# Performance work log

Hardware: AMD Instinct MI355X
Metric: run time of the kernel (lower is better)

## Reference

```python
import jax, jax.numpy as jnp
import numpy as np

B, N, C = 4, 1024, 1024
H, D = 16, 64            # n_heads, head_dim; inner_dim = H*D = C
L = 6                    # n_blocks
FF = 4 * C
SCALE = C ** (-0.5)      # source uses width**-0.5
EPS = 1e-5


def setup_inputs() -> dict:
    key = jax.random.key(0)
    ks = jax.random.split(key, 9)
    s = 0.02
    return {
        "x":     jax.random.normal(ks[0], (B, N, C), dtype=jnp.float32),
        "Wqkv":  jax.random.normal(ks[1], (L, C, 3 * H * D), dtype=jnp.float32) * s,
        "Wout":  jax.random.normal(ks[2], (L, H * D, C), dtype=jnp.float32) * s,
        "bout":  jnp.zeros((L, C), dtype=jnp.float32),
        "W1":    jax.random.normal(ks[3], (L, C, FF), dtype=jnp.float32) * s,
        "b1":    jnp.zeros((L, FF), dtype=jnp.float32),
        "W2":    jax.random.normal(ks[4], (L, FF, C), dtype=jnp.float32) * s,
        "b2":    jnp.zeros((L, C), dtype=jnp.float32),
        "ln1_g": jnp.ones((C,), dtype=jnp.float32),
        "ln1_b": jnp.zeros((C,), dtype=jnp.float32),
        "ln2_g": jnp.ones((C,), dtype=jnp.float32),
        "ln2_b": jnp.zeros((C,), dtype=jnp.float32),
    }


def _layernorm(y, g, b):
    mu = jnp.mean(y, axis=-1, keepdims=True)
    var = jnp.mean(jnp.square(y - mu), axis=-1, keepdims=True)
    return (y - mu) * jax.lax.rsqrt(var + EPS) * g + b


def reference(x, Wqkv, Wout, bout, W1, b1, W2, b2, ln1_g, ln1_b, ln2_g, ln2_b):
    for l in range(L):
        # --- pre-norm multi-head attention (shared LN params across blocks) ---
        h = _layernorm(x, ln1_g, ln1_b)
        qkv = h @ Wqkv[l]                              # [B,N,3HD]
        q, k, v = jnp.split(qkv, 3, axis=-1)
        def heads(t):
            return t.reshape(B, N, H, D).transpose(0, 2, 1, 3)  # [B,H,N,D]
        q, k, v = heads(q), heads(k), heads(v)
        dots = jnp.einsum('bhid,bhjd->bhij', q, k) * SCALE
        attn = jax.nn.softmax(dots, axis=-1)
        o = jnp.einsum('bhij,bhjd->bhid', attn, v)     # [B,H,N,D]
        o = o.transpose(0, 2, 1, 3).reshape(B, N, H * D)
        x = x + (o @ Wout[l] + bout[l])
        # --- pre-norm FFN with exact GELU ---
        h2 = _layernorm(x, ln2_g, ln2_b)
        f = jax.nn.gelu(h2 @ W1[l] + b1[l], approximate=False) @ W2[l] + b2[l]
        x = x + f
    return x
```

## Files before the change

kernel.cpp:

```cpp
#include <hip/hip_runtime.h>
#include <stdint.h>

typedef unsigned short u16;
typedef __bf16  bf16x8 __attribute__((ext_vector_type(8)));
typedef float   f32x4  __attribute__((ext_vector_type(4)));

#define DEVINL __device__ __forceinline__

DEVINL u16 f2bf(float f) {
    union { float f; uint32_t u; } v; v.f = f;
    uint32_t r = v.u + 0x7fffu + ((v.u >> 16) & 1u);
    return (u16)(r >> 16);
}

DEVINL float gelu_exact(float x) {
    return 0.5f * x * (1.0f + erff(x * 0.70710678118654752f));
}

typedef const void __attribute__((address_space(1))) gvoid;
typedef void __attribute__((address_space(3))) lvoid;
DEVINL void gload_lds16(const u16* g, u16* l) {
    __builtin_amdgcn_global_load_lds((gvoid*)g, (lvoid*)l, 16, 0, 0);
}

__global__ __launch_bounds__(256) void k_transpose_conv(
    const float* __restrict__ W, u16* __restrict__ Wt, int K, int N) {
    __shared__ float t[32][33];
    const int n0 = blockIdx.x * 32, k0 = blockIdx.y * 32;
    const int tx = threadIdx.x & 31, ty = threadIdx.x >> 5;
#pragma unroll
    for (int i = 0; i < 4; i++)
        t[ty + i * 8][tx] = W[(size_t)(k0 + ty + i * 8) * N + n0 + tx];
    __syncthreads();
#pragma unroll
    for (int i = 0; i < 4; i++)
        Wt[(size_t)(n0 + ty + i * 8) * K + k0 + tx] = f2bf(t[tx][ty + i * 8]);
}

__global__ __launch_bounds__(256) void k_layernorm(
    const float* __restrict__ x, const float* __restrict__ g,
    const float* __restrict__ b, u16* __restrict__ out) {
    const int row = blockIdx.x, tid = threadIdx.x;
    float4 v = ((const float4*)x)[(size_t)row * 256 + tid];
    float s  = v.x + v.y + v.z + v.w;
    float s2 = v.x * v.x + v.y * v.y + v.z * v.z + v.w * v.w;
#pragma unroll
    for (int off = 32; off > 0; off >>= 1) {
        s  += __shfl_down(s, off);
        s2 += __shfl_down(s2, off);
    }
    __shared__ float rs[4], rs2[4];
    const int wv = tid >> 6;
    if ((tid & 63) == 0) { rs[wv] = s; rs2[wv] = s2; }
    __syncthreads();
    s  = rs[0] + rs[1] + rs[2] + rs[3];
    s2 = rs2[0] + rs2[1] + rs2[2] + rs2[3];
    const float mu  = s * (1.0f / 1024.0f);
    const float var = s2 * (1.0f / 1024.0f) - mu * mu;
    const float rstd = rsqrtf(var + 1e-5f);
    float4 gv = ((const float4*)g)[tid];
    float4 bv = ((const float4*)b)[tid];
    uint2 o;
    u16 a0 = f2bf((v.x - mu) * rstd * gv.x + bv.x);
    u16 a1 = f2bf((v.y - mu) * rstd * gv.y + bv.y);
    u16 a2 = f2bf((v.z - mu) * rstd * gv.z + bv.z);
    u16 a3 = f2bf((v.w - mu) * rstd * gv.w + bv.w);
    o.x = a0 | ((uint32_t)a1 << 16);
    o.y = a2 | ((uint32_t)a3 << 16);
    ((uint2*)out)[(size_t)row * 256 + tid] = o;
}

enum { EPI_BF16 = 0, EPI_F32_BIAS_RES = 1, EPI_BF16_BIAS_GELU = 2 };

template <int EPI>
__global__ __launch_bounds__(256) void k_gemm_bt(
    const u16* __restrict__ A, const u16* __restrict__ Bt,
    void* outp, const float* __restrict__ bias, const float* res,
    int N, int K) {
    __shared__ __align__(16) u16 As[128 * 32];
    __shared__ __align__(16) u16 Bs[128 * 32];
    const int tid  = threadIdx.x;
    const int lane = tid & 63, wv = tid >> 6;
    const int wm = wv >> 1, wn = wv & 1;
    const int lr = lane >> 2, lc = (lane & 3) * 8;
    const int c0 = wv * 2;
    const size_t aRow0 = (size_t)blockIdx.y * 128;
    const size_t bRow0 = (size_t)blockIdx.x * 128;

    f32x4 acc[4][4] = {};
    const int mrow = lane & 15;
    const int koff = (lane >> 4) * 8;
    const int kIters = K >> 5;

    for (int kt = 0; kt < kIters; kt++) {
        const int k0 = kt << 5;
        gload_lds16(A  + (aRow0 + (size_t)(c0 * 16      + lr)) * K + k0 + lc, &As[c0 * 512]);
        gload_lds16(A  + (aRow0 + (size_t)(c0 * 16 + 16 + lr)) * K + k0 + lc, &As[(c0 + 1) * 512]);
        gload_lds16(Bt + (bRow0 + (size_t)(c0 * 16      + lr)) * K + k0 + lc, &Bs[c0 * 512]);
        gload_lds16(Bt + (bRow0 + (size_t)(c0 * 16 + 16 + lr)) * K + k0 + lc, &Bs[(c0 + 1) * 512]);
        __syncthreads();
        bf16x8 af[4], bfv[4];
#pragma unroll
        for (int i = 0; i < 4; i++)
            af[i] = *(const bf16x8*)&As[(wm * 64 + i * 16 + mrow) * 32 + koff];
#pragma unroll
        for (int i = 0; i < 4; i++)
            bfv[i] = *(const bf16x8*)&Bs[(wn * 64 + i * 16 + mrow) * 32 + koff];
#pragma unroll
        for (int mi = 0; mi < 4; mi++)
#pragma unroll
            for (int ni = 0; ni < 4; ni++)
                acc[mi][ni] = __builtin_amdgcn_mfma_f32_16x16x32_bf16(
                    af[mi], bfv[ni], acc[mi][ni], 0, 0, 0);
        __syncthreads();
    }

    const int rr = (lane >> 4) * 4;
    const int cc = lane & 15;
#pragma unroll
    for (int mi = 0; mi < 4; mi++) {
#pragma unroll
        for (int ni = 0; ni < 4; ni++) {
#pragma unroll
            for (int r = 0; r < 4; r++) {
                const size_t row = aRow0 + wm * 64 + mi * 16 + rr + r;
                const size_t col = bRow0 + wn * 64 + ni * 16 + cc;
                const float v = acc[mi][ni][r];
                if (EPI == EPI_BF16) {
                    ((u16*)outp)[row * N + col] = f2bf(v);
                } else if (EPI == EPI_F32_BIAS_RES) {
                    ((float*)outp)[row * N + col] = res[row * N + col] + v + bias[col];
                } else {
                    ((u16*)outp)[row * N + col] = f2bf(gelu_exact(v + bias[col]));
                }
            }
        }
    }
}

__global__ __launch_bounds__(256) void k_vtrans(
    const u16* __restrict__ qkv, u16* __restrict__ vT) {
    __shared__ u16 t[32][33];
    const int bh = blockIdx.z;
    const int b = bh >> 4, h = bh & 15;
    const int n0 = blockIdx.x * 32, d0 = blockIdx.y * 32;
    const int tx = threadIdx.x & 31, ty = threadIdx.x >> 5;
#pragma unroll
    for (int i = 0; i < 4; i++)
        t[ty + i * 8][tx] = qkv[(size_t)(b * 1024 + n0 + ty + i * 8) * 3072 + 2048 + h * 64 + d0 + tx];
    __syncthreads();
#pragma unroll
    for (int i = 0; i < 4; i++)
        vT[(size_t)(bh * 64 + d0 + ty + i * 8) * 1024 + n0 + tx] = t[tx][ty + i * 8];
}

__global__ __launch_bounds__(256) void k_attention(
    const u16* __restrict__ qkv, const u16* __restrict__ vT, u16* __restrict__ o) {
    const int qt = blockIdx.x, h = blockIdx.y, b = blockIdx.z;
    const int tid = threadIdx.x;
    const int lane = tid & 63, wv = tid >> 6;
    const int quad = lane >> 4, l16 = lane & 15;
    __shared__ __align__(16) u16 Ks[64 * 64];
    __shared__ __align__(16) u16 Vs[64 * 64];
    __shared__ __align__(16) u16 Ps[4][16 * 64];
    const int q0 = qt * 64 + wv * 16;

    bf16x8 qa[2];
    {
        const u16* qp = qkv + (size_t)(b * 1024 + q0 + l16) * 3072 + h * 64 + quad * 8;
        qa[0] = *(const bf16x8*)qp;
        qa[1] = *(const bf16x8*)(qp + 32);
    }
    f32x4 oacc[4] = {};
    float mst[4], lst[4];
#pragma unroll
    for (int r = 0; r < 4; r++) { mst[r] = -__builtin_inff(); lst[r] = 0.f; }

    const int tr = tid >> 3, tc = (tid & 7) * 8;
    const size_t kvbase = (size_t)(b * 1024) * 3072 + 1024 + h * 64;
    const size_t vtbase = (size_t)(b * 16 + h) * 64 * 1024;

    for (int j0 = 0; j0 < 1024; j0 += 64) {
        *(uint4*)&Ks[tr * 64 + tc]        = *(const uint4*)&qkv[kvbase + (size_t)(j0 + tr) * 3072 + tc];
        *(uint4*)&Ks[(tr + 32) * 64 + tc] = *(const uint4*)&qkv[kvbase + (size_t)(j0 + tr + 32) * 3072 + tc];
        *(uint4*)&Vs[tr * 64 + tc]        = *(const uint4*)&vT[vtbase + (size_t)tr * 1024 + j0 + tc];
        *(uint4*)&Vs[(tr + 32) * 64 + tc] = *(const uint4*)&vT[vtbase + (size_t)(tr + 32) * 1024 + j0 + tc];
        __syncthreads();

        f32x4 s[4] = {};
#pragma unroll
        for (int nt = 0; nt < 4; nt++) {
            bf16x8 kb0 = *(const bf16x8*)&Ks[(nt * 16 + l16) * 64 + quad * 8];
            bf16x8 kb1 = *(const bf16x8*)&Ks[(nt * 16 + l16) * 64 + quad * 8 + 32];
            s[nt] = __builtin_amdgcn_mfma_f32_16x16x32_bf16(qa[0], kb0, s[nt], 0, 0, 0);
            s[nt] = __builtin_amdgcn_mfma_f32_16x16x32_bf16(qa[1], kb1, s[nt], 0, 0, 0);
        }
#pragma unroll
        for (int r = 0; r < 4; r++) {
            float v0 = s[0][r] * 0.03125f, v1 = s[1][r] * 0.03125f;
            float v2 = s[2][r] * 0.03125f, v3 = s[3][r] * 0.03125f;
            float mx = fmaxf(fmaxf(v0, v1), fmaxf(v2, v3));
#pragma unroll
            for (int off = 1; off < 16; off <<= 1) mx = fmaxf(mx, __shfl_xor(mx, off));
            const float mnew = fmaxf(mst[r], mx);
            const float alpha = __expf(mst[r] - mnew);
            mst[r] = mnew;
            const float p0 = __expf(v0 - mnew), p1 = __expf(v1 - mnew);
            const float p2 = __expf(v2 - mnew), p3 = __expf(v3 - mnew);
            float rsum = p0 + p1 + p2 + p3;
#pragma unroll
            for (int off = 1; off < 16; off <<= 1) rsum += __shfl_xor(rsum, off);
            lst[r] = lst[r] * alpha + rsum;
#pragma unroll
            for (int dt = 0; dt < 4; dt++) oacc[dt][r] *= alpha;
            u16* pr = &Ps[wv][(quad * 4 + r) * 64 + l16];
            pr[0]  = f2bf(p0); pr[16] = f2bf(p1);
            pr[32] = f2bf(p2); pr[48] = f2bf(p3);
        }
        __syncthreads();
        bf16x8 pa0 = *(const bf16x8*)&Ps[wv][l16 * 64 + quad * 8];
        bf16x8 pa1 = *(const bf16x8*)&Ps[wv][l16 * 64 + quad * 8 + 32];
#pragma unroll
        for (int dt = 0; dt < 4; dt++) {
            bf16x8 vb0 = *(const bf16x8*)&Vs[(dt * 16 + l16) * 64 + quad * 8];
            bf16x8 vb1 = *(const bf16x8*)&Vs[(dt * 16 + l16) * 64 + quad * 8 + 32];
            oacc[dt] = __builtin_amdgcn_mfma_f32_16x16x32_bf16(pa0, vb0, oacc[dt], 0, 0, 0);
            oacc[dt] = __builtin_amdgcn_mfma_f32_16x16x32_bf16(pa1, vb1, oacc[dt], 0, 0, 0);
        }
        __syncthreads();
    }
#pragma unroll
    for (int dt = 0; dt < 4; dt++)
#pragma unroll
        for (int r = 0; r < 4; r++) {
            const float v = oacc[dt][r] / lst[r];
            o[(size_t)(b * 1024 + q0 + quad * 4 + r) * 1024 + h * 64 + dt * 16 + l16] = f2bf(v);
        }
}

extern "C" void kernel_launch(void* const* d_in, const int* in_sizes, int n_in,
                              void* d_out, int out_size, void* d_ws, size_t ws_size,
                              hipStream_t stream) {
    const float* x_in = (const float*)d_in[0];
    const float* Wqkv = (const float*)d_in[1];
    const float* Wout = (const float*)d_in[2];
    const float* bout = (const float*)d_in[3];
    const float* W1   = (const float*)d_in[4];
    const float* b1   = (const float*)d_in[5];
    const float* W2   = (const float*)d_in[6];
    const float* b2   = (const float*)d_in[7];
    const float* ln1g = (const float*)d_in[8];
    const float* ln1b = (const float*)d_in[9];
    const float* ln2g = (const float*)d_in[10];
    const float* ln2b = (const float*)d_in[11];
    float* xbuf = (float*)d_out;

    char* p = (char*)d_ws;
    auto carve = [&](size_t elems) -> u16* {
        u16* r = (u16*)p;
        p += ((elems * 2 + 255) & ~(size_t)255);
        return r;
    };
    u16* wq   = carve((size_t)3072 * 1024);
    u16* wo   = carve((size_t)1024 * 1024);
    u16* w1t  = carve((size_t)4096 * 1024);
    u16* w2t  = carve((size_t)1024 * 4096);
    u16* hb   = carve((size_t)4096 * 1024);
    u16* qkvb = carve((size_t)4096 * 3072);
    u16* vtb  = carve((size_t)4096 * 1024);
    u16* ob   = carve((size_t)4096 * 1024);
    u16* gb   = carve((size_t)4096 * 4096);
    if ((size_t)(p - (char*)d_ws) > ws_size) return;

    hipMemcpyAsync(xbuf, x_in, (size_t)4096 * 1024 * 4, hipMemcpyDeviceToDevice, stream);

    for (int l = 0; l < 6; l++) {
        k_transpose_conv<<<dim3(96, 32), 256, 0, stream>>>(Wqkv + (size_t)l * 1024 * 3072, wq, 1024, 3072);
        k_transpose_conv<<<dim3(32, 32), 256, 0, stream>>>(Wout + (size_t)l * 1024 * 1024, wo, 1024, 1024);
        k_transpose_conv<<<dim3(128, 32), 256, 0, stream>>>(W1 + (size_t)l * 1024 * 4096, w1t, 1024, 4096);
        k_transpose_conv<<<dim3(32, 128), 256, 0, stream>>>(W2 + (size_t)l * 4096 * 1024, w2t, 4096, 1024);

        k_layernorm<<<4096, 256, 0, stream>>>(xbuf, ln1g, ln1b, hb);
        k_gemm_bt<EPI_BF16><<<dim3(24, 32), 256, 0, stream>>>(hb, wq, qkvb, nullptr, nullptr, 3072, 1024);
        k_vtrans<<<dim3(32, 2, 64), 256, 0, stream>>>(qkvb, vtb);
        k_attention<<<dim3(16, 16, 4), 256, 0, stream>>>(qkvb, vtb, ob);
        k_gemm_bt<EPI_F32_BIAS_RES><<<dim3(8, 32), 256, 0, stream>>>(ob, wo, xbuf, bout + (size_t)l * 1024, xbuf, 1024, 1024);
        k_layernorm<<<4096, 256, 0, stream>>>(xbuf, ln2g, ln2b, hb);
        k_gemm_bt<EPI_BF16_BIAS_GELU><<<dim3(32, 32), 256, 0, stream>>>(hb, w1t, gb, b1 + (size_t)l * 4096, nullptr, 4096, 1024);
        k_gemm_bt<EPI_F32_BIAS_RES><<<dim3(8, 32), 256, 0, stream>>>(gb, w2t, xbuf, b2 + (size_t)l * 1024, xbuf, 1024, 4096);
    }
}
```

Before: 2.394 ms.

## Split-K with atomic residual add for narrow GEMMs, swizzle LDS tiles

The N=1024 GEMMs (attention output projection and FFN down projection) are split along K across blockIdx.z, 2 and 4 ways. Each split atomically adds its partial into the fp32 residual buffer, and split 0 also adds the bias. This raises the grid from 256 blocks to 512/1024 so more CUs are busy. Separately, the GEMM and attention LDS tiles use XOR swizzles and a padded P buffer to cut bank conflicts. In exchange, fp32 atomics add memory traffic and make the summation order nondeterministic.

```diff
diff --git a/kernel.cpp b/kernel.cpp
--- a/kernel.cpp
+++ b/kernel.cpp
@@ -70,30 +70,34 @@
     ((uint2*)out)[(size_t)row * 256 + tid] = o;
 }
 
-enum { EPI_BF16 = 0, EPI_F32_BIAS_RES = 1, EPI_BF16_BIAS_GELU = 2 };
+enum { EPI_BF16 = 0, EPI_F32_ATOMIC = 1, EPI_BF16_BIAS_GELU = 2 };
 
 template <int EPI>
 __global__ __launch_bounds__(256) void k_gemm_bt(
     const u16* __restrict__ A, const u16* __restrict__ Bt,
-    void* outp, const float* __restrict__ bias, const float* res,
-    int N, int K) {
+    void* outp, const float* __restrict__ bias,
+    int N, int K, int kPer) {
     __shared__ __align__(16) u16 As[128 * 32];
     __shared__ __align__(16) u16 Bs[128 * 32];
     const int tid  = threadIdx.x;
     const int lane = tid & 63, wv = tid >> 6;
     const int wm = wv >> 1, wn = wv & 1;
-    const int lr = lane >> 2, lc = (lane & 3) * 8;
+    const int lr = lane >> 2;
+    const int lc = ((lane & 3) ^ ((lane >> 3) & 3)) * 8;
     const int c0 = wv * 2;
     const size_t aRow0 = (size_t)blockIdx.y * 128;
     const size_t bRow0 = (size_t)blockIdx.x * 128;
+    const int ks = blockIdx.z;
+    const int kBase = ks * kPer;
 
     f32x4 acc[4][4] = {};
     const int mrow = lane & 15;
-    const int koff = (lane >> 4) * 8;
-    const int kIters = K >> 5;
+    const int quad = lane >> 4;
+    const int koff = ((quad ^ ((mrow >> 1) & 3)) << 3);
+    const int kIters = kPer >> 5;
 
     for (int kt = 0; kt < kIters; kt++) {
-        const int k0 = kt << 5;
+        const int k0 = kBase + (kt << 5);
         gload_lds16(A  + (aRow0 + (size_t)(c0 * 16      + lr)) * K + k0 + lc, &As[c0 * 512]);
         gload_lds16(A  + (aRow0 + (size_t)(c0 * 16 + 16 + lr)) * K + k0 + lc, &As[(c0 + 1) * 512]);
         gload_lds16(Bt + (bRow0 + (size_t)(c0 * 16      + lr)) * K + k0 + lc, &Bs[c0 * 512]);
@@ -115,8 +119,8 @@
         __syncthreads();
     }
 
-    const int rr = (lane >> 4) * 4;
-    const int cc = lane & 15;
+    const int rr = quad * 4;
+    const int cc = mrow;
 #pragma unroll
     for (int mi = 0; mi < 4; mi++) {
 #pragma unroll
@@ -128,8 +132,9 @@
                 const float v = acc[mi][ni][r];
                 if (EPI == EPI_BF16) {
                     ((u16*)outp)[row * N + col] = f2bf(v);
-                } else if (EPI == EPI_F32_BIAS_RES) {
-                    ((float*)outp)[row * N + col] = res[row * N + col] + v + bias[col];
+                } else if (EPI == EPI_F32_ATOMIC) {
+                    const float add = (ks == 0) ? v + bias[col] : v;
+                    atomicAdd(&((float*)outp)[row * N + col], add);
                 } else {
                     ((u16*)outp)[row * N + col] = f2bf(gelu_exact(v + bias[col]));
                 }
@@ -162,7 +167,7 @@
     const int quad = lane >> 4, l16 = lane & 15;
     __shared__ __align__(16) u16 Ks[64 * 64];
     __shared__ __align__(16) u16 Vs[64 * 64];
-    __shared__ __align__(16) u16 Ps[4][16 * 64];
+    __shared__ __align__(16) u16 Ps[4][16 * 72];
     const int q0 = qt * 64 + wv * 16;
 
     bf16x8 qa[2];
@@ -176,22 +181,24 @@
 #pragma unroll
     for (int r = 0; r < 4; r++) { mst[r] = -__builtin_inff(); lst[r] = 0.f; }
 
-    const int tr = tid >> 3, tc = (tid & 7) * 8;
+    const int tr = tid >> 3, tc = tid & 7;
+    const int cs = (tc ^ (tr & 7)) * 8;
     const size_t kvbase = (size_t)(b * 1024) * 3072 + 1024 + h * 64;
     const size_t vtbase = (size_t)(b * 16 + h) * 64 * 1024;
 
     for (int j0 = 0; j0 < 1024; j0 += 64) {
-        *(uint4*)&Ks[tr * 64 + tc]        = *(const uint4*)&qkv[kvbase + (size_t)(j0 + tr) * 3072 + tc];
-        *(uint4*)&Ks[(tr + 32) * 64 + tc] = *(const uint4*)&qkv[kvbase + (size_t)(j0 + tr + 32) * 3072 + tc];
-        *(uint4*)&Vs[tr * 64 + tc]        = *(const uint4*)&vT[vtbase + (size_t)tr * 1024 + j0 + tc];
-        *(uint4*)&Vs[(tr + 32) * 64 + tc] = *(const uint4*)&vT[vtbase + (size_t)(tr + 32) * 1024 + j0 + tc];
+        *(uint4*)&Ks[tr * 64 + cs]        = *(const uint4*)&qkv[kvbase + (size_t)(j0 + tr) * 3072 + tc * 8];
+        *(uint4*)&Ks[(tr + 32) * 64 + cs] = *(const uint4*)&qkv[kvbase + (size_t)(j0 + tr + 32) * 3072 + tc * 8];
+        *(uint4*)&Vs[tr * 64 + cs]        = *(const uint4*)&vT[vtbase + (size_t)tr * 1024 + j0 + tc * 8];
+        *(uint4*)&Vs[(tr + 32) * 64 + cs] = *(const uint4*)&vT[vtbase + (size_t)(tr + 32) * 1024 + j0 + tc * 8];
         __syncthreads();
 
         f32x4 s[4] = {};
 #pragma unroll
         for (int nt = 0; nt < 4; nt++) {
-            bf16x8 kb0 = *(const bf16x8*)&Ks[(nt * 16 + l16) * 64 + quad * 8];
-            bf16x8 kb1 = *(const bf16x8*)&Ks[(nt * 16 + l16) * 64 + quad * 8 + 32];
+            const int rk = nt * 16 + l16;
+            bf16x8 kb0 = *(const bf16x8*)&Ks[rk * 64 + ((quad ^ (rk & 7)) * 8)];
+            bf16x8 kb1 = *(const bf16x8*)&Ks[rk * 64 + (((quad + 4) ^ (rk & 7)) * 8)];
             s[nt] = __builtin_amdgcn_mfma_f32_16x16x32_bf16(qa[0], kb0, s[nt], 0, 0, 0);
             s[nt] = __builtin_amdgcn_mfma_f32_16x16x32_bf16(qa[1], kb1, s[nt], 0, 0, 0);
         }
@@ -213,17 +220,18 @@
             lst[r] = lst[r] * alpha + rsum;
 #pragma unroll
             for (int dt = 0; dt < 4; dt++) oacc[dt][r] *= alpha;
-            u16* pr = &Ps[wv][(quad * 4 + r) * 64 + l16];
+            u16* pr = &Ps[wv][(quad * 4 + r) * 72 + l16];
             pr[0]  = f2bf(p0); pr[16] = f2bf(p1);
             pr[32] = f2bf(p2); pr[48] = f2bf(p3);
         }
         __syncthreads();
-        bf16x8 pa0 = *(const bf16x8*)&Ps[wv][l16 * 64 + quad * 8];
-        bf16x8 pa1 = *(const bf16x8*)&Ps[wv][l16 * 64 + quad * 8 + 32];
+        bf16x8 pa0 = *(const bf16x8*)&Ps[wv][l16 * 72 + quad * 8];
+        bf16x8 pa1 = *(const bf16x8*)&Ps[wv][l16 * 72 + quad * 8 + 32];
 #pragma unroll
         for (int dt = 0; dt < 4; dt++) {
-            bf16x8 vb0 = *(const bf16x8*)&Vs[(dt * 16 + l16) * 64 + quad * 8];
-            bf16x8 vb1 = *(const bf16x8*)&Vs[(dt * 16 + l16) * 64 + quad * 8 + 32];
+            const int rv = dt * 16 + l16;
+            bf16x8 vb0 = *(const bf16x8*)&Vs[rv * 64 + ((quad ^ (rv & 7)) * 8)];
+            bf16x8 vb1 = *(const bf16x8*)&Vs[rv * 64 + (((quad + 4) ^ (rv & 7)) * 8)];
             oacc[dt] = __builtin_amdgcn_mfma_f32_16x16x32_bf16(pa0, vb0, oacc[dt], 0, 0, 0);
             oacc[dt] = __builtin_amdgcn_mfma_f32_16x16x32_bf16(pa1, vb1, oacc[dt], 0, 0, 0);
         }
@@ -281,12 +289,12 @@
         k_transpose_conv<<<dim3(32, 128), 256, 0, stream>>>(W2 + (size_t)l * 4096 * 1024, w2t, 4096, 1024);
 
         k_layernorm<<<4096, 256, 0, stream>>>(xbuf, ln1g, ln1b, hb);
-        k_gemm_bt<EPI_BF16><<<dim3(24, 32), 256, 0, stream>>>(hb, wq, qkvb, nullptr, nullptr, 3072, 1024);
+        k_gemm_bt<EPI_BF16><<<dim3(24, 32, 1), 256, 0, stream>>>(hb, wq, qkvb, nullptr, 3072, 1024, 1024);
         k_vtrans<<<dim3(32, 2, 64), 256, 0, stream>>>(qkvb, vtb);
         k_attention<<<dim3(16, 16, 4), 256, 0, stream>>>(qkvb, vtb, ob);
-        k_gemm_bt<EPI_F32_BIAS_RES><<<dim3(8, 32), 256, 0, stream>>>(ob, wo, xbuf, bout + (size_t)l * 1024, xbuf, 1024, 1024);
+        k_gemm_bt<EPI_F32_ATOMIC><<<dim3(8, 32, 2), 256, 0, stream>>>(ob, wo, xbuf, bout + (size_t)l * 1024, 1024, 1024, 512);
         k_layernorm<<<4096, 256, 0, stream>>>(xbuf, ln2g, ln2b, hb);
-        k_gemm_bt<EPI_BF16_BIAS_GELU><<<dim3(32, 32), 256, 0, stream>>>(hb, w1t, gb, b1 + (size_t)l * 4096, nullptr, 4096, 1024);
-        k_gemm_bt<EPI_F32_BIAS_RES><<<dim3(8, 32), 256, 0, stream>>>(gb, w2t, xbuf, b2 + (size_t)l * 1024, xbuf, 1024, 4096);
-    }
-}
+        k_gemm_bt<EPI_BF16_BIAS_GELU><<<dim3(32, 32, 1), 256, 0, stream>>>(hb, w1t, gb, b1 + (size_t)l * 4096, 4096, 1024, 1024);
+        k_gemm_bt<EPI_F32_ATOMIC><<<dim3(8, 32, 4), 256, 0, stream>>>(gb, w2t, xbuf, b2 + (size_t)l * 1024, 1024, 4096, 1024);
+    }
+}
```

After: 2.256 ms. -5.8%, faster.
